# Kernel tuning notes

Hardware: AMD Instinct MI355X
Metric: run time of the kernel (lower is better)

The kernel has to match this reference:

```python
import jax, jax.numpy as jnp
import numpy as np

H = 768          # hidden_size
HH = H // 2      # 384


def setup_inputs() -> dict:
    key = jax.random.key(0)
    ks = jax.random.split(key, 16)
    B, W, E, R = 32, 512, 128, 1024
    inp = {
        "hidden_states": jax.random.normal(ks[0], (B, W, H), dtype=jnp.float32),
        "relation_head": jax.random.randint(ks[1], (B, R), 0, E),
        "relation_tail": jax.random.randint(ks[2], (B, R), 0, E),
        "relation_label": jax.random.randint(ks[3], (B, R), 0, 2),
        "entities_start": jax.random.randint(ks[4], (B, E), 0, W),
        "entities_end": jax.random.randint(ks[5], (B, E), 0, W),
        "entities_label": jax.random.randint(ks[6], (B, E), 0, 3),
        # parameters (torch Linear convention: weight [out, in])
        "entity_emb": jax.random.normal(ks[7], (3, H), dtype=jnp.float32) * 0.02,
        "Wh1": jax.random.normal(ks[8], (H, 2 * H), dtype=jnp.float32) * 0.02,
        "bh1": jnp.zeros((H,), jnp.float32),
        "Wh2": jax.random.normal(ks[9], (HH, H), dtype=jnp.float32) * 0.02,
        "bh2": jnp.zeros((HH,), jnp.float32),
        "Wt1": jax.random.normal(ks[10], (H, 2 * H), dtype=jnp.float32) * 0.02,
        "bt1": jnp.zeros((H,), jnp.float32),
        "Wt2": jax.random.normal(ks[11], (HH, H), dtype=jnp.float32) * 0.02,
        "bt2": jnp.zeros((HH,), jnp.float32),
        "W_bil": jax.random.normal(ks[12], (2, HH, HH), dtype=jnp.float32) * 0.02,
        "W_lin": jax.random.normal(ks[13], (2, 2 * HH), dtype=jnp.float32) * 0.02,
        "b_lin": jnp.zeros((2,), jnp.float32),
    }
    return inp


def _ffnn(x, W1, b1, W2, b2):
    # two-layer MLP with ReLU (dropout is identity in eval mode)
    h = jax.nn.relu(jnp.einsum('brd,hd->brh', x, W1) + b1)
    return jax.nn.relu(jnp.einsum('brh,oh->bro', h, W2) + b2)


def reference(hidden_states, relation_head, relation_tail, relation_label,
              entities_start, entities_end, entities_label,
              entity_emb, Wh1, bh1, Wh2, bh2, Wt1, bt1, Wt2, bt2,
              W_bil, W_lin, b_lin):
    # gather per-relation entity info: [B, R]
    head_index = jnp.take_along_axis(entities_start, relation_head, axis=1)
    head_label = jnp.take_along_axis(entities_label, relation_head, axis=1)
    tail_index = jnp.take_along_axis(entities_start, relation_tail, axis=1)
    tail_label = jnp.take_along_axis(entities_label, relation_tail, axis=1)

    # gather token reprs: [B, R, H]
    head_tok = jnp.take_along_axis(hidden_states, head_index[:, :, None], axis=1)
    tail_tok = jnp.take_along_axis(hidden_states, tail_index[:, :, None], axis=1)

    head_repr = jnp.concatenate([head_tok, entity_emb[head_label]], axis=-1)  # [B,R,2H]
    tail_repr = jnp.concatenate([tail_tok, entity_emb[tail_label]], axis=-1)

    heads = _ffnn(head_repr, Wh1, bh1, Wh2, bh2)  # [B,R,HH]
    tails = _ffnn(tail_repr, Wt1, bt1, Wt2, bt2)

    # biaffine: bilinear + linear on concat
    bil = jnp.einsum('bri,oij,brj->bro', heads, W_bil, tails)
    lin = jnp.einsum('brc,oc->bro', jnp.concatenate([heads, tails], axis=-1), W_lin) + b_lin
    logits = bil + lin  # [B, R, 2]

    # per-doc mean CE summed over docs
    logp = jax.nn.log_softmax(logits, axis=-1)
    nll = -jnp.take_along_axis(logp, relation_label[:, :, None], axis=-1)[..., 0]  # [B,R]
    loss = jnp.sum(jnp.mean(nll, axis=1))
    return loss
```

## Files before the change

### kernel.cpp

```cpp
#include <hip/hip_runtime.h>
#include <math.h>

typedef unsigned short u16;
typedef __bf16 bf16x8 __attribute__((ext_vector_type(8)));
typedef float f32x4 __attribute__((ext_vector_type(4)));

#define B_ 32
#define W_ 512
#define H_ 768
#define HH_ 384
#define E_ 128
#define R_ 1024
#define BE_ 4096
#define K1_ 1536
#define BKK 64

__device__ __forceinline__ u16 f2bf(float f) {
  unsigned u = __float_as_uint(f);
  u = (u + 0x7fffu + ((u >> 16) & 1u)) >> 16;
  return (u16)u;
}
__device__ __forceinline__ float bf2f(u16 u) {
  return __uint_as_float(((unsigned)u) << 16);
}
__device__ __forceinline__ void gload_lds16(const void* g, void* l) {
  __builtin_amdgcn_global_load_lds(
      (__attribute__((address_space(1))) void*)(g),
      (__attribute__((address_space(3))) void*)(l), 16, 0, 0);
}

#define NBLK_W1 1152
#define NBLK_P  1152
#define NBLK_X  512

__global__ __launch_bounds__(256) void prep_all(
    const float* __restrict__ Wh1, const float* __restrict__ Wt1,
    const float* __restrict__ bh1, const float* __restrict__ bt1,
    const float* __restrict__ emb,
    const float* __restrict__ hs, const int* __restrict__ ent_start,
    u16* __restrict__ W1c, float* __restrict__ P, u16* __restrict__ X)
{
  const int blk = blockIdx.x;
  const int tid = threadIdx.x;

  if (blk < NBLK_W1) {
    const int i = blk * 256 + tid;
    int row = i / 192, c = i % 192;
    const float4* src = (const float4*)((row < 768)
        ? (Wh1 + (size_t)row * K1_) : (Wt1 + (size_t)(row - 768) * K1_));
    float4 v = src[c];
    ushort4 o; o.x = f2bf(v.x); o.y = f2bf(v.y); o.z = f2bf(v.z); o.w = f2bf(v.w);
    ((ushort4*)W1c)[i] = o;
  } else if (blk < NBLK_W1 + NBLK_P) {
    const int w = (blk - NBLK_W1) * 4 + (tid >> 6);
    const int lane = tid & 63;
    const int l = w / K1_;
    const int n = w - l * K1_;
    const float* wrow = (n < 768) ? (Wh1 + (size_t)n * K1_ + 768)
                                  : (Wt1 + (size_t)(n - 768) * K1_ + 768);
    const float bb = (n < 768) ? bh1[n] : bt1[n - 768];
    const float* ev = emb + (size_t)l * H_;
    float s = 0.f;
#pragma unroll
    for (int t = 0; t < 12; ++t) {
      int d = lane + 64 * t;
      s += ev[d] * wrow[d];
    }
#pragma unroll
    for (int off = 32; off; off >>= 1) s += __shfl_down(s, off);
    if (lane == 0) P[(size_t)l * K1_ + n] = s + bb;
  } else {
    const int g = blk - (NBLK_W1 + NBLK_P);
    if (tid < 192) {
#pragma unroll
      for (int e = 0; e < 8; ++e) {
        const int be = g * 8 + e;
        int b = be >> 7;
        int start = ent_start[be];
        float4 v = ((const float4*)(hs + ((size_t)b * W_ + start) * H_))[tid];
        ushort4 o; o.x = f2bf(v.x); o.y = f2bf(v.y); o.z = f2bf(v.z); o.w = f2bf(v.w);
        ((ushort4*)(X + (size_t)be * H_))[tid] = o;
      }
    }
  }
}

template<int TBM, int TBN, int DEPTH, int MINB>
__global__ __launch_bounds__(256, MINB) void gemm_bf16(
    const u16* __restrict__ A, int lda,
    const u16* __restrict__ Wt,
    const float* __restrict__ bias,
    u16* __restrict__ C, int ldc,
    int K, int do_relu, int half_n, int aoff,
    const float* __restrict__ rowBias,
    const int* __restrict__ rowLabel, int ldP,
    int ngemm,
    const float* __restrict__ tWh2, const float* __restrict__ tWt2,
    const float* __restrict__ tWbil,
    const float* __restrict__ tbh2, const float* __restrict__ tbt2,
    u16* __restrict__ tW2c, u16* __restrict__ tWb, float* __restrict__ tb2cat,
    const u16* __restrict__ linSrc, const float* __restrict__ W_lin,
    float* __restrict__ linHT, float* __restrict__ outZ)
{
  constexpr int FM = TBM / 32;
  constexpr int FN = TBN / 32;
  constexpr int AU = TBM / 8;
  constexpr int UNITS = (TBM + TBN) / 8;
  constexpr int UPW = UNITS / 4;
  constexpr int BUFB = (TBM + TBN) * 128;

  __shared__ char smem[DEPTH * BUFB];

  const int tid = threadIdx.x;
  const int id  = blockIdx.y * gridDim.x + blockIdx.x;

  if (id >= ngemm) {
    const int tailid = id - ngemm;
    const int ntail  = gridDim.x * gridDim.y - ngemm;
    if (tW2c) {
      for (int i = tailid * 256 + tid; i < 221376; i += ntail * 256) {
        if (i < 147456) {
          float4 v = (i < 73728) ? ((const float4*)tWh2)[i]
                                 : ((const float4*)tWt2)[i - 73728];
          ushort4 o; o.x = f2bf(v.x); o.y = f2bf(v.y); o.z = f2bf(v.z); o.w = f2bf(v.w);
          ((ushort4*)tW2c)[i] = o;
        } else if (i < 221184) {
          int j = i - 147456;
          float4 v = ((const float4*)tWbil)[j];
          ushort4 o; o.x = f2bf(v.x); o.y = f2bf(v.y); o.z = f2bf(v.z); o.w = f2bf(v.w);
          ((ushort4*)tWb)[j] = o;
        } else {
          int j = i - 221184;
          ((float4*)tb2cat)[j] = (j < 96) ? ((const float4*)tbh2)[j]
                                          : ((const float4*)tbt2)[j - 96];
        }
      }
    } else if (linHT) {
      if (tailid == 0 && tid == 0) outZ[0] = 0.f;
      const int wave  = tailid * 4 + (tid >> 6);
      const int nwave = ntail * 4;
      const int lane  = tid & 63;
      for (int be = wave; be < BE_; be += nwave) {
        const ushort4* src = (const ushort4*)(linSrc + (size_t)be * 768);
        float s0 = 0.f, s1 = 0.f, s2 = 0.f, s3 = 0.f;
#pragma unroll
        for (int rd = 0; rd < 3; ++rd) {
          const int idx4 = rd * 64 + lane;
          const int c = idx4 * 4;
          ushort4 v4 = src[idx4];
          float4 w0 = *(const float4*)(W_lin + c);
          float4 w1 = *(const float4*)(W_lin + 768 + c);
          float d0 = bf2f(v4.x)*w0.x + bf2f(v4.y)*w0.y + bf2f(v4.z)*w0.z + bf2f(v4.w)*w0.w;
          float d1 = bf2f(v4.x)*w1.x + bf2f(v4.y)*w1.y + bf2f(v4.z)*w1.z + bf2f(v4.w)*w1.w;
          if (c < 384) { s0 += d0; s1 += d1; }
          else         { s2 += d0; s3 += d1; }
        }
#pragma unroll
        for (int off = 32; off; off >>= 1) {
          s0 += __shfl_down(s0, off);
          s1 += __shfl_down(s1, off);
          s2 += __shfl_down(s2, off);
          s3 += __shfl_down(s3, off);
        }
        if (lane == 0) {
          float4 v = {s0, s1, s2, s3};
          *(float4*)(linHT + (size_t)be * 4) = v;
        }
      }
    }
    return;
  }

  const int q = ngemm >> 3, r = ngemm & 7;
  const int xcd = id & 7, idx = id >> 3;
  const int wgid = (xcd < r ? xcd * (q + 1) : r * (q + 1) + (xcd - r) * q) + idx;
  const int nbx = gridDim.x;
  const int bn = (wgid % nbx) * TBN;
  const int bm = (wgid / nbx) * TBM;

  const int wid  = tid >> 6;
  const int lane = tid & 63;
  const int wm = (wid >> 1) * (TBM / 2);
  const int wn = (wid & 1) * (TBN / 2);

  const int a0 = (half_n && bn >= half_n) ? aoff : 0;

  const int srow = lane >> 3;
  const int sk8  = (lane & 7) ^ srow;
  const u16* gA = A  + (size_t)(bm + srow) * lda + a0 + 8 * sk8;
  const u16* gB = Wt + (size_t)(bn + srow) * K + 8 * sk8;

  const int frow = lane & 15;
  const int fk8  = lane >> 4;

  f32x4 acc[FM][FN] = {};

  auto stage = [&](int buf, int k0) {
    char* base = smem + buf * BUFB;
#pragma unroll
    for (int i = 0; i < UPW; ++i) {
      const int u = wid * UPW + i;
      if (u < AU)
        gload_lds16(gA + (size_t)(u * 8) * lda + k0, base + u * 1024);
      else
        gload_lds16(gB + (size_t)((u - AU) * 8) * K + k0, base + u * 1024);
    }
  };

  const int nt = K / BKK;
  stage(0, 0);

  for (int t = 0; t < nt; ++t) {
    const int cur = t % DEPTH;
    if (t + 1 < nt) {
      stage((t + 1) % DEPTH, (t + 1) * BKK);
      asm volatile("s_waitcnt vmcnt(%0)" :: "n"(UPW) : "memory");
    } else {
      asm volatile("s_waitcnt vmcnt(0)" ::: "memory");
    }
    __builtin_amdgcn_s_barrier();

    char* As = smem + cur * BUFB;
    char* Bs = As + TBM * 128;
#pragma unroll
    for (int kh = 0; kh < 2; ++kh) {
      bf16x8 a[FM], b[FN];
#pragma unroll
      for (int m = 0; m < FM; ++m) {
        const int row  = wm + m * 16 + frow;
        const int slot = (kh * 4 + fk8) ^ (row & 7);
        a[m] = *(const bf16x8*)(As + row * 128 + slot * 16);
      }
#pragma unroll
      for (int n = 0; n < FN; ++n) {
        const int row  = wn + n * 16 + frow;
        const int slot = (kh * 4 + fk8) ^ (row & 7);
        b[n] = *(const bf16x8*)(Bs + row * 128 + slot * 16);
      }
#pragma unroll
      for (int m = 0; m < FM; ++m)
#pragma unroll
        for (int n = 0; n < FN; ++n)
          acc[m][n] = __builtin_amdgcn_mfma_f32_16x16x32_bf16(
              a[m], b[n], acc[m][n], 0, 0, 0);
    }

    if (DEPTH == 2 && t + 1 < nt)
      __builtin_amdgcn_s_barrier();
  }

  int lbl[FM][4];
  if (rowLabel) {
#pragma unroll
    for (int m = 0; m < FM; ++m)
#pragma unroll
      for (int r2 = 0; r2 < 4; ++r2)
        lbl[m][r2] = rowLabel[bm + wm + m * 16 + fk8 * 4 + r2];
  }

#pragma unroll
  for (int n = 0; n < FN; ++n) {
    const int col = bn + wn + n * 16 + frow;
    const float bv = bias ? bias[col] : 0.f;
    float p0 = 0.f, p1 = 0.f, p2 = 0.f;
    if (rowLabel) {
      p0 = rowBias[col];
      p1 = rowBias[ldP + col];
      p2 = rowBias[2 * ldP + col];
    }
#pragma unroll
    for (int m = 0; m < FM; ++m) {
#pragma unroll
      for (int r2 = 0; r2 < 4; ++r2) {
        const int row = bm + wm + m * 16 + fk8 * 4 + r2;
        float v = acc[m][n][r2] + bv;
        if (rowLabel) {
          int l = lbl[m][r2];
          v += (l == 0) ? p0 : ((l == 1) ? p1 : p2);
        }
        if (do_relu) v = fmaxf(v, 0.f);
        C[(size_t)row * ldc + col] = f2bf(v);
      }
    }
  }
}

__global__ __launch_bounds__(256, 2) void gemm_S_ce(
    const u16* __restrict__ Hcat, const u16* __restrict__ U,
    const float* __restrict__ linHT, const float* __restrict__ b_lin,
    const int* __restrict__ rel_head, const int* __restrict__ rel_tail,
    const int* __restrict__ rel_label, float* __restrict__ out)
{
  __shared__ char smem[3 * 16384];
  float* Sl  = (float*)smem;
  float* red = (float*)(smem + 64 * 65 * 4);

  const int xcd = blockIdx.x & 7, idx = blockIdx.x >> 3;
  const int wgid = xcd * 32 + idx;
  const int bn = (wgid & 3) * 64;
  const int zz = wgid >> 2;
  const int z  = zz >> 1;
  const int bm = (zz & 1) * 64;

  const int tid  = threadIdx.x;
  const int wid  = tid >> 6;
  const int lane = tid & 63;
  const int srow = lane >> 3;
  const int sk8  = (lane & 7) ^ srow;

  auto stage = [&](int buf, int k0) {
    char* base = smem + buf * 16384;
#pragma unroll
    for (int i = 0; i < 4; ++i) {
      const int u = wid * 4 + i;
      if (u < 8) {
        const int row = z*128 + bm + u*8 + srow;
        gload_lds16(Hcat + (size_t)row * 768 + k0 + 8*sk8, base + u*1024);
      } else {
        const int row = bn + (u - 8)*8 + srow;
        gload_lds16(U + (size_t)z*98304 + (size_t)row * 384 + k0 + 8*sk8,
                    base + u*1024);
      }
    }
  };

  const int wm = (wid >> 1) * 32;
  const int wn = (wid & 1) * 32;
  const int frow = lane & 15;
  const int fk8  = lane >> 4;

  f32x4 acc[2][2] = {};

  stage(0, 0);

  for (int t = 0; t < 6; ++t) {
    const int cur = t % 3;
    if (t + 1 < 6) {
      stage((t + 1) % 3, (t + 1) * BKK);
      asm volatile("s_waitcnt vmcnt(4)" ::: "memory");
    } else {
      asm volatile("s_waitcnt vmcnt(0)" ::: "memory");
    }
    __builtin_amdgcn_s_barrier();

    char* As = smem + cur * 16384;
    char* Bs = As + 8192;
#pragma unroll
    for (int kh = 0; kh < 2; ++kh) {
      bf16x8 a[2], b[2];
#pragma unroll
      for (int m = 0; m < 2; ++m) {
        const int row  = wm + m*16 + frow;
        const int slot = (kh*4 + fk8) ^ (row & 7);
        a[m] = *(const bf16x8*)(As + row*128 + slot*16);
      }
#pragma unroll
      for (int n = 0; n < 2; ++n) {
        const int row  = wn + n*16 + frow;
        const int slot = (kh*4 + fk8) ^ (row & 7);
        b[n] = *(const bf16x8*)(Bs + row*128 + slot*16);
      }
#pragma unroll
      for (int m = 0; m < 2; ++m)
#pragma unroll
        for (int n = 0; n < 2; ++n)
          acc[m][n] = __builtin_amdgcn_mfma_f32_16x16x32_bf16(
              a[m], b[n], acc[m][n], 0, 0, 0);
    }
  }

  const int o = frow & 1;
  const float blv = b_lin[o];
#pragma unroll
  for (int n = 0; n < 2; ++n) {
    const int lc = wn + n*16 + frow;
    const int e2 = (bn + lc) >> 1;
    const float lt = linHT[(size_t)(z*128 + e2) * 4 + 2 + o];
#pragma unroll
    for (int m = 0; m < 2; ++m) {
#pragma unroll
      for (int r = 0; r < 4; ++r) {
        const int lr = wm + m*16 + fk8*4 + r;
        const float lh = linHT[(size_t)(z*128 + bm + lr) * 4 + o];
        Sl[lr * 65 + lc] = acc[m][n][r] + lh + lt + blv;
      }
    }
  }
  __syncthreads();

  float nllsum = 0.f;
#pragma unroll
  for (int j = 0; j < 4; ++j) {
    const int i = z * 1024 + tid + 256 * j;
    const int rh = rel_head[i];
    const int rt = rel_tail[i];
    const int lab = rel_label[i];
    if ((unsigned)(rh - bm) < 64u && (unsigned)(rt*2 - bn) < 64u) {
      const float l0 = Sl[(rh - bm) * 65 + (rt*2 - bn)];
      const float l1 = Sl[(rh - bm) * 65 + (rt*2 - bn) + 1];
      const float mx = fmaxf(l0, l1);
      const float lse = mx + logf(expf(l0 - mx) + expf(l1 - mx));
      nllsum += lse - (lab == 0 ? l0 : l1);
    }
  }
#pragma unroll
  for (int off = 32; off; off >>= 1) nllsum += __shfl_down(nllsum, off);
  if (lane == 0) red[wid] = nllsum;
  __syncthreads();
  if (tid == 0)
    atomicAdd(out, (red[0] + red[1] + red[2] + red[3]) * (1.0f / R_));
}

extern "C" void kernel_launch(void* const* d_in, const int* in_sizes, int n_in,
                              void* d_out, int out_size, void* d_ws, size_t ws_size,
                              hipStream_t stream)
{
  const float* hs        = (const float*)d_in[0];
  const int*   rel_head  = (const int*)  d_in[1];
  const int*   rel_tail  = (const int*)  d_in[2];
  const int*   rel_label = (const int*)  d_in[3];
  const int*   ent_start = (const int*)  d_in[4];
  const int*   ent_label = (const int*)  d_in[6];
  const float* emb   = (const float*)d_in[7];
  const float* Wh1   = (const float*)d_in[8];
  const float* bh1   = (const float*)d_in[9];
  const float* Wh2   = (const float*)d_in[10];
  const float* bh2   = (const float*)d_in[11];
  const float* Wt1   = (const float*)d_in[12];
  const float* bt1   = (const float*)d_in[13];
  const float* Wt2   = (const float*)d_in[14];
  const float* bt2   = (const float*)d_in[15];
  const float* Wbil  = (const float*)d_in[16];
  const float* W_lin = (const float*)d_in[17];
  const float* b_lin = (const float*)d_in[18];
  float* out = (float*)d_out;

  u16* X    = (u16*)d_ws;
  u16* H1   = X    + (size_t)BE_ * H_;
  u16* Hcat = H1   + (size_t)BE_ * K1_;
  u16* U    = Hcat + (size_t)BE_ * H_;
  u16* W1c  = U    + (size_t)BE_ * H_;
  u16* W2c  = W1c  + (size_t)K1_ * H_;
  u16* Wb   = W2c  + (size_t)H_ * H_;
  float* b2cat = (float*)(Wb + (size_t)H_ * HH_);
  float* P     = b2cat + H_;
  float* linHT = P + 3*K1_;

  prep_all<<<dim3(NBLK_W1 + NBLK_P + NBLK_X), dim3(256), 0, stream>>>(
      Wh1, Wt1, bh1, bt1, emb, hs, ent_start, W1c, P, X);

  gemm_bf16<128, 128, 2, 2><<<dim3(12, 34), dim3(256), 0, stream>>>(
      X, H_, W1c, (const float*)nullptr, H1, K1_, H_, 1, 0, 0,
      P, ent_label, K1_, 384,
      Wh2, Wt2, Wbil, bh2, bt2, W2c, Wb, b2cat,
      (const u16*)nullptr, (const float*)nullptr, (float*)nullptr, (float*)nullptr);

  gemm_bf16<128, 96, 3, 1><<<dim3(8, 32), dim3(256), 0, stream>>>(
      H1, K1_, W2c, b2cat, Hcat, H_, H_, 1, HH_, H_,
      (const float*)nullptr, (const int*)nullptr, 0, 256,
      (const float*)nullptr, (const float*)nullptr, (const float*)nullptr,
      (const float*)nullptr, (const float*)nullptr,
      (u16*)nullptr, (u16*)nullptr, (float*)nullptr,
      (const u16*)nullptr, (const float*)nullptr, (float*)nullptr, (float*)nullptr);

  gemm_bf16<128, 96, 2, 2><<<dim3(8, 49), dim3(256), 0, stream>>>(
      Hcat + HH_, H_, Wb, (const float*)nullptr, U, H_, HH_, 0, 0, 0,
      (const float*)nullptr, (const int*)nullptr, 0, 256,
      (const float*)nullptr, (const float*)nullptr, (const float*)nullptr,
      (const float*)nullptr, (const float*)nullptr,
      (u16*)nullptr, (u16*)nullptr, (float*)nullptr,
      Hcat, W_lin, linHT, out);

  gemm_S_ce<<<dim3(256), dim3(256), 0, stream>>>(
      Hcat, U, linHT, b_lin, rel_head, rel_tail, rel_label, out);
}
```

Before: 61.16 us.

## Switch the three FFNN and bilinear GEMMs from bf16 to scaled fp8 MFMA

Converts weights and activations to fp8 (e4m3) with fixed power-of-two scales and runs the first three GEMMs on the fp8 16x16x32 MFMA, with the scale undone in the epilogue. The K tile doubles to 128 bytes per row, which halves the number of k-iterations, and the pipeline is fixed at two buffers. The second GEMM also writes an fp8 copy of the tail half so the bilinear GEMM can read fp8. This halves operand bandwidth and LDS traffic, at the cost of accuracy risk from fp8 quantization and a hand-written software conversion routine.

```diff
diff --git a/kernel.cpp b/kernel.cpp
--- a/kernel.cpp
+++ b/kernel.cpp
@@ -2,6 +2,8 @@
 #include <math.h>
 
 typedef unsigned short u16;
+typedef unsigned char u8;
+typedef long long i64;
 typedef __bf16 bf16x8 __attribute__((ext_vector_type(8)));
 typedef float f32x4 __attribute__((ext_vector_type(4)));
 
@@ -13,7 +15,7 @@
 #define R_ 1024
 #define BE_ 4096
 #define K1_ 1536
-#define BKK 64
+#define BKE 128
 
 __device__ __forceinline__ u16 f2bf(float f) {
   unsigned u = __float_as_uint(f);
@@ -22,6 +24,27 @@
 }
 __device__ __forceinline__ float bf2f(u16 u) {
   return __uint_as_float(((unsigned)u) << 16);
+}
+__device__ __forceinline__ u8 f2fp8(float f) {
+  unsigned su = (__float_as_uint(f) >> 24) & 0x80u;
+  float a = fabsf(f);
+  if (a >= 448.f) return (u8)(su | 0x7Eu);
+  if (a < 0.015625f) {
+    int q = (int)rintf(a * 512.f);
+    return (u8)(su | (unsigned)q);
+  }
+  unsigned u = __float_as_uint(a);
+  u += 0x7FFFFu + ((u >> 20) & 1u);
+  unsigned e = (u >> 23) - 120u;
+  unsigned m = (u >> 20) & 7u;
+  if (e >= 16u) return (u8)(su | 0x7Eu);
+  return (u8)(su | (e << 3) | m);
+}
+__device__ __forceinline__ uchar4 f4_to_fp8x4(float4 v, float s) {
+  uchar4 o;
+  o.x = f2fp8(v.x * s); o.y = f2fp8(v.y * s);
+  o.z = f2fp8(v.z * s); o.w = f2fp8(v.w * s);
+  return o;
 }
 __device__ __forceinline__ void gload_lds16(const void* g, void* l) {
   __builtin_amdgcn_global_load_lds(
@@ -38,7 +61,7 @@
     const float* __restrict__ bh1, const float* __restrict__ bt1,
     const float* __restrict__ emb,
     const float* __restrict__ hs, const int* __restrict__ ent_start,
-    u16* __restrict__ W1c, float* __restrict__ P, u16* __restrict__ X)
+    u8* __restrict__ W1c, float* __restrict__ P, u8* __restrict__ X)
 {
   const int blk = blockIdx.x;
   const int tid = threadIdx.x;
@@ -48,9 +71,7 @@
     int row = i / 192, c = i % 192;
     const float4* src = (const float4*)((row < 768)
         ? (Wh1 + (size_t)row * K1_) : (Wt1 + (size_t)(row - 768) * K1_));
-    float4 v = src[c];
-    ushort4 o; o.x = f2bf(v.x); o.y = f2bf(v.y); o.z = f2bf(v.z); o.w = f2bf(v.w);
-    ((ushort4*)W1c)[i] = o;
+    ((uchar4*)W1c)[i] = f4_to_fp8x4(src[c], 16.f);
   } else if (blk < NBLK_W1 + NBLK_P) {
     const int w = (blk - NBLK_W1) * 4 + (tid >> 6);
     const int lane = tid & 63;
@@ -78,27 +99,26 @@
         int b = be >> 7;
         int start = ent_start[be];
         float4 v = ((const float4*)(hs + ((size_t)b * W_ + start) * H_))[tid];
-        ushort4 o; o.x = f2bf(v.x); o.y = f2bf(v.y); o.z = f2bf(v.z); o.w = f2bf(v.w);
-        ((ushort4*)(X + (size_t)be * H_))[tid] = o;
-      }
-    }
-  }
-}
-
-template<int TBM, int TBN, int DEPTH, int MINB>
-__global__ __launch_bounds__(256, MINB) void gemm_bf16(
-    const u16* __restrict__ A, int lda,
-    const u16* __restrict__ Wt,
-    const float* __restrict__ bias,
+        ((uchar4*)(X + (size_t)be * H_))[tid] = f4_to_fp8x4(v, 1.f);
+      }
+    }
+  }
+}
+
+template<int TBM, int TBN, int MINB>
+__global__ __launch_bounds__(256, MINB) void gemm_fp8(
+    const u8* __restrict__ A, int lda,
+    const u8* __restrict__ Wt, int K,
+    const float* __restrict__ bias, float oscale,
     u16* __restrict__ C, int ldc,
-    int K, int do_relu, int half_n, int aoff,
-    const float* __restrict__ rowBias,
-    const int* __restrict__ rowLabel, int ldP,
+    u8* __restrict__ C8, int ldc8, int c8off, float c8scale,
+    int do_relu, int half_n, int aoff,
+    const float* __restrict__ rowBias, const int* __restrict__ rowLabel, int ldP,
     int ngemm,
     const float* __restrict__ tWh2, const float* __restrict__ tWt2,
     const float* __restrict__ tWbil,
     const float* __restrict__ tbh2, const float* __restrict__ tbt2,
-    u16* __restrict__ tW2c, u16* __restrict__ tWb, float* __restrict__ tb2cat,
+    u8* __restrict__ tW2c, u8* __restrict__ tWb, float* __restrict__ tb2cat,
     const u16* __restrict__ linSrc, const float* __restrict__ W_lin,
     float* __restrict__ linHT, float* __restrict__ outZ)
 {
@@ -109,7 +129,7 @@
   constexpr int UPW = UNITS / 4;
   constexpr int BUFB = (TBM + TBN) * 128;
 
-  __shared__ char smem[DEPTH * BUFB];
+  __shared__ char smem[2 * BUFB];
 
   const int tid = threadIdx.x;
   const int id  = blockIdx.y * gridDim.x + blockIdx.x;
@@ -122,13 +142,10 @@
         if (i < 147456) {
           float4 v = (i < 73728) ? ((const float4*)tWh2)[i]
                                  : ((const float4*)tWt2)[i - 73728];
-          ushort4 o; o.x = f2bf(v.x); o.y = f2bf(v.y); o.z = f2bf(v.z); o.w = f2bf(v.w);
-          ((ushort4*)tW2c)[i] = o;
+          ((uchar4*)tW2c)[i] = f4_to_fp8x4(v, 16.f);
         } else if (i < 221184) {
           int j = i - 147456;
-          float4 v = ((const float4*)tWbil)[j];
-          ushort4 o; o.x = f2bf(v.x); o.y = f2bf(v.y); o.z = f2bf(v.z); o.w = f2bf(v.w);
-          ((ushort4*)tWb)[j] = o;
+          ((uchar4*)tWb)[j] = f4_to_fp8x4(((const float4*)tWbil)[j], 16.f);
         } else {
           int j = i - 221184;
           ((float4*)tb2cat)[j] = (j < 96) ? ((const float4*)tbh2)[j]
@@ -187,8 +204,8 @@
 
   const int srow = lane >> 3;
   const int sk8  = (lane & 7) ^ srow;
-  const u16* gA = A  + (size_t)(bm + srow) * lda + a0 + 8 * sk8;
-  const u16* gB = Wt + (size_t)(bn + srow) * K + 8 * sk8;
+  const u8* gA = A  + (size_t)(bm + srow) * lda + a0 + 16 * sk8;
+  const u8* gB = Wt + (size_t)(bn + srow) * K + 16 * sk8;
 
   const int frow = lane & 15;
   const int fk8  = lane >> 4;
@@ -207,13 +224,13 @@
     }
   };
 
-  const int nt = K / BKK;
+  const int nt = K / BKE;
   stage(0, 0);
 
   for (int t = 0; t < nt; ++t) {
-    const int cur = t % DEPTH;
+    const int cur = t & 1;
     if (t + 1 < nt) {
-      stage((t + 1) % DEPTH, (t + 1) * BKK);
+      stage(cur ^ 1, (t + 1) * BKE);
       asm volatile("s_waitcnt vmcnt(%0)" :: "n"(UPW) : "memory");
     } else {
       asm volatile("s_waitcnt vmcnt(0)" ::: "memory");
@@ -223,29 +240,29 @@
     char* As = smem + cur * BUFB;
     char* Bs = As + TBM * 128;
 #pragma unroll
-    for (int kh = 0; kh < 2; ++kh) {
-      bf16x8 a[FM], b[FN];
+    for (int kh = 0; kh < 4; ++kh) {
+      i64 a[FM], b[FN];
 #pragma unroll
       for (int m = 0; m < FM; ++m) {
-        const int row  = wm + m * 16 + frow;
-        const int slot = (kh * 4 + fk8) ^ (row & 7);
-        a[m] = *(const bf16x8*)(As + row * 128 + slot * 16);
+        const int row = wm + m * 16 + frow;
+        const int ch  = (kh * 2 + (fk8 >> 1)) ^ (row & 7);
+        a[m] = *(const i64*)(As + row * 128 + ch * 16 + (fk8 & 1) * 8);
       }
 #pragma unroll
       for (int n = 0; n < FN; ++n) {
-        const int row  = wn + n * 16 + frow;
-        const int slot = (kh * 4 + fk8) ^ (row & 7);
-        b[n] = *(const bf16x8*)(Bs + row * 128 + slot * 16);
+        const int row = wn + n * 16 + frow;
+        const int ch  = (kh * 2 + (fk8 >> 1)) ^ (row & 7);
+        b[n] = *(const i64*)(Bs + row * 128 + ch * 16 + (fk8 & 1) * 8);
       }
 #pragma unroll
       for (int m = 0; m < FM; ++m)
 #pragma unroll
         for (int n = 0; n < FN; ++n)
-          acc[m][n] = __builtin_amdgcn_mfma_f32_16x16x32_bf16(
+          acc[m][n] = __builtin_amdgcn_mfma_f32_16x16x32_fp8_fp8(
               a[m], b[n], acc[m][n], 0, 0, 0);
     }
 
-    if (DEPTH == 2 && t + 1 < nt)
+    if (t + 1 < nt)
       __builtin_amdgcn_s_barrier();
   }
 
@@ -273,13 +290,15 @@
 #pragma unroll
       for (int r2 = 0; r2 < 4; ++r2) {
         const int row = bm + wm + m * 16 + fk8 * 4 + r2;
-        float v = acc[m][n][r2] + bv;
+        float v = acc[m][n][r2] * oscale + bv;
         if (rowLabel) {
           int l = lbl[m][r2];
           v += (l == 0) ? p0 : ((l == 1) ? p1 : p2);
         }
         if (do_relu) v = fmaxf(v, 0.f);
-        C[(size_t)row * ldc + col] = f2bf(v);
+        if (C)  C[(size_t)row * ldc + col] = f2bf(v);
+        if (C8 && col >= c8off)
+          C8[(size_t)row * ldc8 + (col - c8off)] = f2fp8(v * c8scale);
       }
     }
   }
@@ -336,7 +355,7 @@
   for (int t = 0; t < 6; ++t) {
     const int cur = t % 3;
     if (t + 1 < 6) {
-      stage((t + 1) % 3, (t + 1) * BKK);
+      stage((t + 1) % 3, (t + 1) * 64);
       asm volatile("s_waitcnt vmcnt(4)" ::: "memory");
     } else {
       asm volatile("s_waitcnt vmcnt(0)" ::: "memory");
@@ -435,40 +454,44 @@
   const float* b_lin = (const float*)d_in[18];
   float* out = (float*)d_out;
 
-  u16* X    = (u16*)d_ws;
-  u16* H1   = X    + (size_t)BE_ * H_;
-  u16* Hcat = H1   + (size_t)BE_ * K1_;
+  u8*  X    = (u8*)d_ws;
+  u8*  H1   = X    + (size_t)BE_ * H_;
+  u8*  THt  = H1   + (size_t)BE_ * K1_;
+  u8*  W1c  = THt  + (size_t)BE_ * HH_;
+  u8*  W2c  = W1c  + (size_t)K1_ * H_;
+  u8*  Wb   = W2c  + (size_t)H_ * H_;
+  u16* Hcat = (u16*)(Wb + (size_t)H_ * HH_);
   u16* U    = Hcat + (size_t)BE_ * H_;
-  u16* W1c  = U    + (size_t)BE_ * H_;
-  u16* W2c  = W1c  + (size_t)K1_ * H_;
-  u16* Wb   = W2c  + (size_t)H_ * H_;
-  float* b2cat = (float*)(Wb + (size_t)H_ * HH_);
+  float* b2cat = (float*)(U + (size_t)BE_ * H_);
   float* P     = b2cat + H_;
   float* linHT = P + 3*K1_;
 
   prep_all<<<dim3(NBLK_W1 + NBLK_P + NBLK_X), dim3(256), 0, stream>>>(
       Wh1, Wt1, bh1, bt1, emb, hs, ent_start, W1c, P, X);
 
-  gemm_bf16<128, 128, 2, 2><<<dim3(12, 34), dim3(256), 0, stream>>>(
-      X, H_, W1c, (const float*)nullptr, H1, K1_, H_, 1, 0, 0,
-      P, ent_label, K1_, 384,
+  gemm_fp8<128, 128, 2><<<dim3(12, 34), dim3(256), 0, stream>>>(
+      X, H_, W1c, H_, (const float*)nullptr, 1.f/16.f,
+      (u16*)nullptr, 0, H1, K1_, 0, 1.f,
+      1, 0, 0, P, ent_label, K1_, 384,
       Wh2, Wt2, Wbil, bh2, bt2, W2c, Wb, b2cat,
       (const u16*)nullptr, (const float*)nullptr, (float*)nullptr, (float*)nullptr);
 
-  gemm_bf16<128, 96, 3, 1><<<dim3(8, 32), dim3(256), 0, stream>>>(
-      H1, K1_, W2c, b2cat, Hcat, H_, H_, 1, HH_, H_,
-      (const float*)nullptr, (const int*)nullptr, 0, 256,
+  gemm_fp8<128, 96, 2><<<dim3(8, 32), dim3(256), 0, stream>>>(
+      H1, K1_, W2c, H_, b2cat, 1.f/16.f,
+      Hcat, H_, THt, HH_, HH_, 4.f,
+      1, HH_, H_, (const float*)nullptr, (const int*)nullptr, 0, 256,
       (const float*)nullptr, (const float*)nullptr, (const float*)nullptr,
       (const float*)nullptr, (const float*)nullptr,
-      (u16*)nullptr, (u16*)nullptr, (float*)nullptr,
+      (u8*)nullptr, (u8*)nullptr, (float*)nullptr,
       (const u16*)nullptr, (const float*)nullptr, (float*)nullptr, (float*)nullptr);
 
-  gemm_bf16<128, 96, 2, 2><<<dim3(8, 49), dim3(256), 0, stream>>>(
-      Hcat + HH_, H_, Wb, (const float*)nullptr, U, H_, HH_, 0, 0, 0,
-      (const float*)nullptr, (const int*)nullptr, 0, 256,
+  gemm_fp8<128, 96, 2><<<dim3(8, 49), dim3(256), 0, stream>>>(
+      THt, HH_, Wb, HH_, (const float*)nullptr, 1.f/64.f,
+      U, H_, (u8*)nullptr, 0, 0, 1.f,
+      0, 0, 0, (const float*)nullptr, (const int*)nullptr, 0, 256,
       (const float*)nullptr, (const float*)nullptr, (const float*)nullptr,
       (const float*)nullptr, (const float*)nullptr,
-      (u16*)nullptr, (u16*)nullptr, (float*)nullptr,
+      (u8*)nullptr, (u8*)nullptr, (float*)nullptr,
       Hcat, W_lin, linHT, out);
 
   gemm_S_ce<<<dim3(256), dim3(256), 0, stream>>>(
```

New measurement: 80.28 us. 1.31x slower.
